# Performance work log

Measured on AMD Instinct MI355X. Metric: run time of the kernel, lower is better.

The kernel has to match this reference:

```python
import jax, jax.numpy as jnp
import numpy as np

N = 50000      # nodes
E = 600000     # edges
IN = 128       # input_dim
HID = 128      # hidden_dim
OUT = 128      # output_dim
H = 4          # heads
D = OUT // H   # head dim
R = 4          # rel_num
L = 2          # n_layer
M = 10000      # len(idx)
EPS = 1e-5


def setup_inputs() -> dict:
    key = jax.random.key(0)
    ks = jax.random.split(key, 16)
    f = jax.random.normal
    inp = {
        "x": f(ks[0], (N, IN), jnp.float32),
        "proj_w": f(ks[1], (IN, HID), jnp.float32) / np.sqrt(IN).astype(np.float32),
        "proj_b": jnp.zeros((HID,), jnp.float32),
        "bn_gamma": jnp.ones((HID,), jnp.float32),
        "bn_beta": jnp.zeros((HID,), jnp.float32),
        # per-layer HGTConv params (stacked on leading L axis; layer0 in=HID, layer1 in=OUT, equal here)
        "q_w": f(ks[2], (L, HID, OUT), jnp.float32) / np.sqrt(HID).astype(np.float32),
        "q_b": jnp.zeros((L, OUT), jnp.float32),
        "k_w": f(ks[3], (L, HID, OUT), jnp.float32) / np.sqrt(HID).astype(np.float32),
        "k_b": jnp.zeros((L, OUT), jnp.float32),
        "v_w": f(ks[4], (L, HID, OUT), jnp.float32) / np.sqrt(HID).astype(np.float32),
        "v_b": jnp.zeros((L, OUT), jnp.float32),
        "a_w": f(ks[5], (L, OUT, OUT), jnp.float32) / np.sqrt(OUT).astype(np.float32),
        "a_b": jnp.zeros((L, OUT), jnp.float32),
        "skip": jnp.ones((L,), jnp.float32),
        "a_rel": f(ks[6], (L, R, H, D, D), jnp.float32) / np.sqrt(D).astype(np.float32),
        "m_rel": f(ks[7], (L, R, H, D, D), jnp.float32) / np.sqrt(D).astype(np.float32),
        "p_rel": jnp.ones((L, R, H), jnp.float32),
        "edge_index": jax.random.randint(ks[8], (2, E), 0, N, dtype=jnp.int32),
        "edge_type": jax.random.randint(ks[9], (E,), 0, R, dtype=jnp.int32),
        "idx": jax.random.randint(ks[10], (M,), 0, N, dtype=jnp.int32),
    }
    return inp


def _hgt_forward(x, proj_w, proj_b, bn_gamma, bn_beta, q_w, q_b, k_w, k_b, v_w, v_b,
                 a_w, a_b, skip, a_rel, m_rel, p_rel, edge_index, edge_type, idx):
    # proj + BatchNorm1d (training-mode batch statistics, biased variance)
    h = x @ proj_w + proj_b
    mu = h.mean(axis=0)
    var = jnp.mean((h - mu) ** 2, axis=0)
    h = (h - mu) * jax.lax.rsqrt(var + EPS) * bn_gamma + bn_beta

    src, dst = edge_index[0], edge_index[1]          # message from src(j) to dst(i)
    seg = dst * R + edge_type                        # per-(dst, relation) softmax segments
    scale = np.float32(1.0 / np.sqrt(D))

    for l in range(L):
        q = (h @ q_w[l] + q_b[l]).reshape(N, H, D)
        k = (h @ k_w[l] + k_b[l]).reshape(N, H, D)
        v = (h @ v_w[l] + v_b[l]).reshape(N, H, D)
        # relation-specific key/value transforms for every node/relation: [N,R,H,D]
        k_all = jnp.einsum('nhd,rhde->nrhe', k, a_rel[l])
        v_all = jnp.einsum('nhd,rhde->nrhe', v, m_rel[l])
        k_e = k_all[src, edge_type]                  # [E,H,D]
        v_e = v_all[src, edge_type]                  # [E,H,D]
        score = jnp.sum(q[dst] * k_e, axis=-1) * p_rel[l][edge_type] * scale  # [E,H]
        # per-relation segment softmax over incoming edges of each dst node
        smax = jax.ops.segment_max(score, seg, num_segments=N * R)
        e = jnp.exp(score - smax[seg])
        denom = jax.ops.segment_sum(e, seg, num_segments=N * R)
        alpha = e / denom[seg]                        # [E,H]
        out = jax.ops.segment_sum(alpha[..., None] * v_e, dst, num_segments=N)
        out = out.reshape(N, OUT)
        out = jax.nn.gelu(out, approximate=False) @ a_w[l] + a_b[l]
        b = jax.nn.sigmoid(skip[l])                   # learned skip gate
        h = b * out + (1.0 - b) * h                   # dims match -> residual mix
    return h[idx]


def reference(x, proj_w, proj_b, bn_gamma, bn_beta, q_w, q_b, k_w, k_b, v_w, v_b,
              a_w, a_b, skip, a_rel, m_rel, p_rel, edge_index, edge_type, idx):
    return _hgt_forward(x, proj_w, proj_b, bn_gamma, bn_beta, q_w, q_b, k_w, k_b,
                        v_w, v_b, a_w, a_b, skip, a_rel, m_rel, p_rel,
                        edge_index, edge_type, idx)
```

## Files before the change

### kernel.cpp

```cpp
#include <hip/hip_runtime.h>
#include <math.h>

#define NN 50000
#define EE 600000
#define MOUT 10000
#define DEGCAP 384
#define NT4 (NN * 4)

typedef short bf16x8 __attribute__((ext_vector_type(8)));
typedef float f32x4 __attribute__((ext_vector_type(4)));

__device__ __forceinline__ unsigned short f2bf(float x) {
    unsigned int u = __float_as_uint(x);
    u = (u + 0x7FFFu + ((u >> 16) & 1u)) >> 16;
    return (unsigned short)u;
}
__device__ __forceinline__ float bf2f(unsigned int b) {
    return __uint_as_float(b << 16);
}

__global__ __launch_bounds__(256) void prep_kernel(
    const float* __restrict__ proj_w, const float* __restrict__ a_w,
    const float* __restrict__ q_w, const float* __restrict__ q_b,
    const float* __restrict__ a_rel,
    const float* __restrict__ k_w, const float* __restrict__ k_b,
    const float* __restrict__ v_w, const float* __restrict__ v_b,
    const float* __restrict__ m_rel, const float* __restrict__ p_rel,
    const float* __restrict__ x,
    unsigned short* __restrict__ wt_pa, unsigned short* __restrict__ qkvw,
    float* __restrict__ fbias, unsigned short* __restrict__ msg_wt,
    unsigned short* __restrict__ x_bf, int* __restrict__ cnt,
    float* __restrict__ stats)
{
    const int b = blockIdx.x, t = threadIdx.x;
    if (b < 192) {
        int wi = b >> 6;
        int flat = (b & 63) * 256 + t;
        int n = flat >> 7, c = flat & 127;
        const float* src = (wi == 0) ? proj_w : (wi == 1) ? a_w : a_w + 16384;
        wt_pa[(size_t)wi * 16384 + n * 128 + c] = f2bf(src[c * 128 + n]);
    } else if (b < 960) {
        int q = b - 192;
        int l = q >= 384 ? 1 : 0;
        int flat = (q - l * 384) * 256 + t;
        int nrow = flat >> 7, c = flat & 127;
        unsigned short* wt = qkvw + (size_t)l * 98304;
        float* fb = fbias + l * 768;
        if (nrow < 512) {
            int r = nrow >> 7, hh = (nrow >> 5) & 3, d = nrow & 31;
            float prl = p_rel[l * 16 + r * 4 + hh] * 0.17677669529663687f;
            const float* qwc = q_w + (size_t)l * 16384 + c * 128 + hh * 32;
            const float* ar  = a_rel + (size_t)(l * 4 + r) * 4096 + hh * 1024 + d * 32;
            float s = 0.f;
            #pragma unroll 8
            for (int e = 0; e < 32; ++e) s += qwc[e] * ar[e];
            wt[(size_t)nrow * 128 + c] = f2bf(s * prl);
            if (c == 0) {
                const float* qb = q_b + l * 128 + hh * 32;
                float bb = 0.f;
                #pragma unroll 8
                for (int e = 0; e < 32; ++e) bb += qb[e] * ar[e];
                fb[nrow] = bb * prl;
            }
        } else {
            int j = nrow - 512;
            int tt = j >> 2, s = j & 3;
            int col = 2 * tt + (s & 1);
            const float* w  = (s < 2) ? k_w : v_w;
            const float* bb = (s < 2) ? k_b : v_b;
            wt[(size_t)nrow * 128 + c] = f2bf(w[(size_t)l * 16384 + c * 128 + col]);
            if (c == 0) fb[nrow] = bb[l * 128 + col];
        }
    } else if (b < 1472) {
        int q = b - 960;
        int l = q >= 256 ? 1 : 0;
        int flat = (q - l * 256) * 256 + t;
        int n = flat >> 9, kk = flat & 511;
        int h = n >> 5, e = n & 31;
        int r = kk >> 7, h2 = (kk >> 5) & 3, d = kk & 31;
        float val = (h2 == h) ? m_rel[(size_t)(l * 4 + r) * 4096 + h * 1024 + d * 32 + e] : 0.f;
        msg_wt[(size_t)l * 65536 + (size_t)n * 512 + kk] = f2bf(val);
    } else if (b < 7722) {
        int i = (b - 1472) * 256 + t;
        if (i < NN * 32) {
            float4 v = ((const float4*)x)[i];
            uint2 pk;
            pk.x = (unsigned int)f2bf(v.x) | ((unsigned int)f2bf(v.y) << 16);
            pk.y = (unsigned int)f2bf(v.z) | ((unsigned int)f2bf(v.w) << 16);
            ((uint2*)x_bf)[i] = pk;
        }
    } else {
        int i = (b - 7722) * 256 + t;
        if (i < NT4) cnt[i] = 0;
        if (i < 256) stats[i] = 0.f;
    }
}

__global__ __launch_bounds__(256) void hist_kernel(const int* __restrict__ ei,
    const int* __restrict__ et, int* __restrict__ cnt, int E)
{
    int e = blockIdx.x * 256 + threadIdx.x;
    if (e < E) atomicAdd(&cnt[ei[E + e] * 4 + et[e]], 1);
}

__global__ __launch_bounds__(256) void scan_block_kernel(const int* __restrict__ cnt,
    int* __restrict__ excl, int* __restrict__ bsum, int n)
{
    __shared__ int tmp[256];
    int i = blockIdx.x * 256 + threadIdx.x;
    int v = (i < n) ? cnt[i] : 0;
    tmp[threadIdx.x] = v;
    __syncthreads();
    for (int ofs = 1; ofs < 256; ofs <<= 1) {
        int t = (threadIdx.x >= ofs) ? tmp[threadIdx.x - ofs] : 0;
        __syncthreads();
        tmp[threadIdx.x] += t;
        __syncthreads();
    }
    if (i < n) excl[i] = tmp[threadIdx.x] - v;
    if (threadIdx.x == 255) bsum[blockIdx.x] = tmp[255];
}

__global__ __launch_bounds__(256) void scan_add_kernel(int* __restrict__ excl,
    const int* __restrict__ bsum, int* __restrict__ fill,
    int* __restrict__ maskz, int n, int total)
{
    __shared__ int red[256];
    const int b = blockIdx.x;
    int partial = 0;
    for (int j = threadIdx.x; j < b; j += 256) partial += bsum[j];
    red[threadIdx.x] = partial;
    __syncthreads();
    for (int ofs = 128; ofs > 0; ofs >>= 1) {
        if (threadIdx.x < ofs) red[threadIdx.x] += red[threadIdx.x + ofs];
        __syncthreads();
    }
    int prefix = red[0];
    int i = b * 256 + threadIdx.x;
    if (i < n) {
        int o = excl[i] + prefix;
        excl[i] = o;
        fill[i] = o;
    }
    if (i < 12500) maskz[i] = 0;
    if (b == 0 && threadIdx.x == 0) excl[n] = total;
}

__global__ __launch_bounds__(256) void scatter_kernel(const int* __restrict__ ei,
    const int* __restrict__ et, int* __restrict__ fill, int* __restrict__ pack,
    const int* __restrict__ idxp, unsigned char* __restrict__ mask, int Mo, int E)
{
    int e = blockIdx.x * 256 + threadIdx.x;
    if (e >= E) return;
    int seg = ei[E + e] * 4 + et[e];
    int p = atomicAdd(&fill[seg], 1);
    pack[p] = ei[e];
    if (e < Mo) mask[idxp[e]] = 1;
}

__global__ __launch_bounds__(256) void projstats_kernel(
    const unsigned short* __restrict__ A, const unsigned short* __restrict__ Wt,
    const float* __restrict__ bias, unsigned short* __restrict__ Cb,
    float* __restrict__ stats, int M)
{
    __shared__ unsigned short As[128 * 40];
    __shared__ unsigned short Bs[128 * 40];
    const int t = threadIdx.x;
    const int wave = t >> 6, lane = t & 63;
    const int quad = lane >> 4, l16 = lane & 15;
    const int row0 = blockIdx.x * 128;
    const int wr = (wave & 1) * 64, wc = (wave >> 1) * 64;
    const int sr = t >> 1, sc = (t & 1) * 16;
    const int grow = row0 + sr;

    f32x4 acc[4][4];
    #pragma unroll
    for (int i = 0; i < 4; ++i)
        #pragma unroll
        for (int j = 0; j < 4; ++j)
            acc[i][j] = (f32x4){0.f, 0.f, 0.f, 0.f};

    uint4 av0 = make_uint4(0,0,0,0), av1 = av0, bv0, bv1;
    if (grow < M) {
        const uint4* ap = (const uint4*)(A + (size_t)grow * 128 + sc);
        av0 = ap[0]; av1 = ap[1];
    }
    {
        const uint4* bp = (const uint4*)(Wt + (size_t)sr * 128 + sc);
        bv0 = bp[0]; bv1 = bp[1];
    }
    for (int it = 0; it < 4; ++it) {
        __syncthreads();
        *(uint4*)(As + sr * 40 + sc)     = av0;
        *(uint4*)(As + sr * 40 + sc + 8) = av1;
        *(uint4*)(Bs + sr * 40 + sc)     = bv0;
        *(uint4*)(Bs + sr * 40 + sc + 8) = bv1;
        __syncthreads();
        if (it + 1 < 4) {
            int kb = (it + 1) * 32;
            if (grow < M) {
                const uint4* ap = (const uint4*)(A + (size_t)grow * 128 + kb + sc);
                av0 = ap[0]; av1 = ap[1];
            }
            const uint4* bp = (const uint4*)(Wt + (size_t)sr * 128 + kb + sc);
            bv0 = bp[0]; bv1 = bp[1];
        }
        bf16x8 af[4], bfr[4];
        #pragma unroll
        for (int f = 0; f < 4; ++f) {
            af[f]  = *(const bf16x8*)(As + (wr + f * 16 + l16) * 40 + quad * 8);
            bfr[f] = *(const bf16x8*)(Bs + (wc + f * 16 + l16) * 40 + quad * 8);
        }
        #pragma unroll
        for (int fr = 0; fr < 4; ++fr)
            #pragma unroll
            for (int fc = 0; fc < 4; ++fc)
                acc[fr][fc] = __builtin_amdgcn_mfma_f32_16x16x32_bf16(
                    af[fr], bfr[fc], acc[fr][fc], 0, 0, 0);
    }

    #pragma unroll
    for (int fc = 0; fc < 4; ++fc) {
        const int col = wc + fc * 16 + l16;
        const float bv = bias[col];
        float s = 0.f, s2 = 0.f;
        #pragma unroll
        for (int fr = 0; fr < 4; ++fr)
            #pragma unroll
            for (int reg = 0; reg < 4; ++reg) {
                int row = row0 + wr + fr * 16 + quad * 4 + reg;
                float val = acc[fr][fc][reg] + bv;
                if (row < M) {
                    Cb[(size_t)row * 128 + col] = f2bf(val);
                    s += val; s2 += val * val;
                }
            }
        s  += __shfl_xor(s, 16);  s  += __shfl_xor(s, 32);
        s2 += __shfl_xor(s2, 16); s2 += __shfl_xor(s2, 32);
        if (quad == 0) {
            atomicAdd(&stats[col], s);
            atomicAdd(&stats[128 + col], s2);
        }
    }
}

__global__ __launch_bounds__(256) void bnqkv_kernel(
    const unsigned short* __restrict__ hb, const float* __restrict__ stats,
    const float* __restrict__ gamma, const float* __restrict__ beta,
    const unsigned short* __restrict__ qkvw, const float* __restrict__ fbias,
    unsigned short* __restrict__ hn, unsigned short* __restrict__ qkv, int M)
{
    __shared__ unsigned short hS[128 * 136];
    __shared__ unsigned short Bs[128 * 40];
    __shared__ float mulS[128], addS[128];
    const int t = threadIdx.x;
    const int row0 = blockIdx.x * 128;
    if (t < 128) {
        float invN = 1.f / 50000.f;
        float mu = stats[t] * invN;
        float var = stats[128 + t] * invN - mu * mu;
        float ml = rsqrtf(var + 1e-5f) * gamma[t];
        mulS[t] = ml;
        addS[t] = beta[t] - mu * ml;
    }
    __syncthreads();
    #pragma unroll
    for (int u = 0; u < 8; ++u) {
        int li = t + u * 256;
        int row = li >> 4, c0 = (li & 15) * 8;
        uint4 pk = make_uint4(0, 0, 0, 0);
        if (row0 + row < M)
            pk = ((const uint4*)(hb + (size_t)(row0 + row) * 128))[li & 15];
        unsigned int w[4] = {pk.x, pk.y, pk.z, pk.w};
        uint4 o;
        unsigned int ov[4];
        #pragma unroll
        for (int g = 0; g < 4; ++g) {
            int c = c0 + g * 2;
            float a0 = bf2f(w[g] & 0xFFFFu) * mulS[c]     + addS[c];
            float a1 = bf2f(w[g] >> 16)     * mulS[c + 1] + addS[c + 1];
            ov[g] = (unsigned int)f2bf(a0) | ((unsigned int)f2bf(a1) << 16);
        }
        o.x = ov[0]; o.y = ov[1]; o.z = ov[2]; o.w = ov[3];
        *(uint4*)(hS + row * 136 + c0) = o;
        if (row0 + row < M)
            ((uint4*)(hn + (size_t)(row0 + row) * 128))[li & 15] = o;
    }
    __syncthreads();

    const int wave = t >> 6, lane = t & 63;
    const int quad = lane >> 4, l16 = lane & 15;
    const int wr = (wave & 1) * 64, wcl = (wave >> 1) * 64;
    const int sr = t >> 1, scc = (t & 1) * 16;
    for (int ch = 0; ch < 6; ++ch) {
        f32x4 acc[4][4];
        #pragma unroll
        for (int i = 0; i < 4; ++i)
            #pragma unroll
            for (int j = 0; j < 4; ++j)
                acc[i][j] = (f32x4){0.f, 0.f, 0.f, 0.f};
        for (int it = 0; it < 4; ++it) {
            __syncthreads();
            const uint4* bp = (const uint4*)(qkvw + (size_t)(ch * 128 + sr) * 128 + it * 32 + scc);
            *(uint4*)(Bs + sr * 40 + scc)     = bp[0];
            *(uint4*)(Bs + sr * 40 + scc + 8) = bp[1];
            __syncthreads();
            bf16x8 af[4], bfr[4];
            #pragma unroll
            for (int f = 0; f < 4; ++f) {
                af[f]  = *(const bf16x8*)(hS + (wr + f * 16 + l16) * 136 + it * 32 + quad * 8);
                bfr[f] = *(const bf16x8*)(Bs + (wcl + f * 16 + l16) * 40 + quad * 8);
            }
            #pragma unroll
            for (int fr = 0; fr < 4; ++fr)
                #pragma unroll
                for (int fc = 0; fc < 4; ++fc)
                    acc[fr][fc] = __builtin_amdgcn_mfma_f32_16x16x32_bf16(
                        af[fr], bfr[fc], acc[fr][fc], 0, 0, 0);
        }
        float b4[4];
        #pragma unroll
        for (int fc = 0; fc < 4; ++fc)
            b4[fc] = fbias[ch * 128 + wcl + fc * 16 + l16];
        #pragma unroll
        for (int fr = 0; fr < 4; ++fr)
            #pragma unroll
            for (int reg = 0; reg < 4; ++reg) {
                int row = row0 + wr + fr * 16 + quad * 4 + reg;
                if (row >= M) continue;
                #pragma unroll
                for (int fc = 0; fc < 4; ++fc) {
                    int col = ch * 128 + wcl + fc * 16 + l16;
                    qkv[(size_t)row * 768 + col] = f2bf(acc[fr][fc][reg] + b4[fc]);
                }
            }
    }
}

__global__ __launch_bounds__(256) void agg_fused_kernel(
    const unsigned short* __restrict__ qkv,
    const unsigned short* __restrict__ qbuf, int qpitch,
    const int* __restrict__ off4, const int* __restrict__ pack,
    const int* __restrict__ rowmap, unsigned short* __restrict__ aggb, int count)
{
    __shared__ int spack[4][DEGCAP];
    const int wv = threadIdx.x >> 6;
    const int lane = threadIdx.x & 63;
    const int unit = blockIdx.x * 4 + wv;
    if (unit >= count) return;
    const int node = rowmap ? __builtin_amdgcn_readfirstlane(rowmap[unit]) : unit;

    int off_r[5];
    #pragma unroll
    for (int i = 0; i < 5; ++i)
        off_r[i] = __builtin_amdgcn_readfirstlane(off4[node * 4 + i]);
    const int beg = off_r[0];
    const int deg = off_r[4] - beg;
    const bool cached = deg <= DEGCAP;

    const unsigned int* qrow = (const unsigned int*)(qbuf + (size_t)unit * qpitch);

    if (cached) {
        for (int i = lane; i < deg; i += 64) spack[wv][i] = pack[beg + i];
        asm volatile("s_waitcnt vmcnt(0) lgkmcnt(0)" ::: "memory");
    }

    unsigned int outw[4];
    for (int r = 0; r < 4; ++r) {
        unsigned int qu = qrow[r * 64 + lane];
        float qx = bf2f(qu & 0xFFFFu);
        float qy = bf2f(qu >> 16);
        float den = 0.f, ax = 0.f, ay = 0.f;

        if (cached) {
            const int rb = off_r[r] - beg, re = off_r[r + 1] - beg;
            for (int i = rb; i < re; i += 4) {
                unsigned int ku[4], vu[4];
                #pragma unroll
                for (int j = 0; j < 4; ++j) {
                    int ii = i + j; if (ii >= re) ii = re - 1;
                    int src = spack[wv][ii];
                    uint2 kv = *(const uint2*)(qkv + (size_t)src * 768 + 512 + lane * 4);
                    ku[j] = kv.x; vu[j] = kv.y;
                }
                float p[4];
                #pragma unroll
                for (int j = 0; j < 4; ++j)
                    p[j] = qx * bf2f(ku[j] & 0xFFFFu) + qy * bf2f(ku[j] >> 16);
                #pragma unroll
                for (int j = 0; j < 4; ++j) {
                    p[j] += __shfl_xor(p[j], 1); p[j] += __shfl_xor(p[j], 2);
                    p[j] += __shfl_xor(p[j], 4); p[j] += __shfl_xor(p[j], 8);
                }
                #pragma unroll
                for (int j = 0; j < 4; ++j) {
                    float s = fminf(fmaxf(p[j], -80.f), 80.f);
                    float e = __expf(s);
                    if (i + j >= re) e = 0.f;
                    den += e;
                    ax += e * bf2f(vu[j] & 0xFFFFu);
                    ay += e * bf2f(vu[j] >> 16);
                }
            }
        } else {
            for (int pp = off_r[r]; pp < off_r[r + 1]; ++pp) {
                int src = __builtin_amdgcn_readfirstlane(pack[pp]);
                uint2 kv = *(const uint2*)(qkv + (size_t)src * 768 + 512 + lane * 4);
                float p0 = qx * bf2f(kv.x & 0xFFFFu) + qy * bf2f(kv.x >> 16);
                p0 += __shfl_xor(p0, 1); p0 += __shfl_xor(p0, 2);
                p0 += __shfl_xor(p0, 4); p0 += __shfl_xor(p0, 8);
                float e = __expf(fminf(fmaxf(p0, -80.f), 80.f));
                den += e;
                ax += e * bf2f(kv.y & 0xFFFFu);
                ay += e * bf2f(kv.y >> 16);
            }
        }
        float inv = den > 0.f ? 1.f / den : 0.f;
        outw[r] = (unsigned int)f2bf(ax * inv) | ((unsigned int)f2bf(ay * inv) << 16);
    }
    unsigned int* op = (unsigned int*)(aggb + (size_t)unit * 512);
    #pragma unroll
    for (int r = 0; r < 4; ++r) op[r * 64 + lane] = outw[r];
}

__global__ __launch_bounds__(256) void mlpqkv_kernel(
    const unsigned short* __restrict__ A, const unsigned short* __restrict__ W3t,
    const unsigned short* __restrict__ AWt, const float* __restrict__ a_bias,
    const float* __restrict__ skipv, const unsigned short* __restrict__ hres,
    const unsigned short* __restrict__ qkvw1, const float* __restrict__ fbias1,
    const unsigned char* __restrict__ mask,
    unsigned short* __restrict__ h1, unsigned short* __restrict__ qkv, int M)
{
    __shared__ unsigned short As[128 * 40];
    __shared__ unsigned short Bs[128 * 40];
    __shared__ unsigned short msgS[128 * 136];
    const int t = threadIdx.x;
    const int wave = t >> 6, lane = t & 63;
    const int quad = lane >> 4, l16 = lane & 15;
    const int row0 = blockIdx.x * 128;
    const int wr = (wave & 1) * 64, wcl = (wave >> 1) * 64;
    const int sr = t >> 1, scc = (t & 1) * 16;
    const int grow = row0 + sr;
    const bool rvalid = grow < M;

    f32x4 acc[4][4];
    #pragma unroll
    for (int i = 0; i < 4; ++i)
        #pragma unroll
        for (int j = 0; j < 4; ++j)
            acc[i][j] = (f32x4){0.f, 0.f, 0.f, 0.f};

    uint4 av0 = make_uint4(0,0,0,0), av1 = av0, bv0, bv1;
    if (rvalid) {
        const uint4* ap = (const uint4*)(A + (size_t)grow * 512 + scc);
        av0 = ap[0]; av1 = ap[1];
    }
    {
        const uint4* bp = (const uint4*)(W3t + (size_t)sr * 512 + scc);
        bv0 = bp[0]; bv1 = bp[1];
    }
    for (int it = 0; it < 16; ++it) {
        __syncthreads();
        *(uint4*)(As + sr * 40 + scc)     = av0;
        *(uint4*)(As + sr * 40 + scc + 8) = av1;
        *(uint4*)(Bs + sr * 40 + scc)     = bv0;
        *(uint4*)(Bs + sr * 40 + scc + 8) = bv1;
        __syncthreads();
        if (it + 1 < 16) {
            int kb = (it + 1) * 32;
            if (rvalid) {
                const uint4* ap = (const uint4*)(A + (size_t)grow * 512 + kb + scc);
                av0 = ap[0]; av1 = ap[1];
            }
            const uint4* bp = (const uint4*)(W3t + (size_t)sr * 512 + kb + scc);
            bv0 = bp[0]; bv1 = bp[1];
        }
        bf16x8 af[4], bfr[4];
        #pragma unroll
        for (int f = 0; f < 4; ++f) {
            af[f]  = *(const bf16x8*)(As + (wr + f * 16 + l16) * 40 + quad * 8);
            bfr[f] = *(const bf16x8*)(Bs + (wcl + f * 16 + l16) * 40 + quad * 8);
        }
        #pragma unroll
        for (int fr = 0; fr < 4; ++fr)
            #pragma unroll
            for (int fc = 0; fc < 4; ++fc)
                acc[fr][fc] = __builtin_amdgcn_mfma_f32_16x16x32_bf16(
                    af[fr], bfr[fc], acc[fr][fc], 0, 0, 0);
    }

    #pragma unroll
    for (int fr = 0; fr < 4; ++fr)
        #pragma unroll
        for (int reg = 0; reg < 4; ++reg) {
            int rl = wr + fr * 16 + quad * 4 + reg;
            #pragma unroll
            for (int fc = 0; fc < 4; ++fc) {
                int col = wcl + fc * 16 + l16;
                float v = acc[fr][fc][reg];
                float gl = 0.5f * v * (1.f + erff(v * 0.70710678118654752f));
                msgS[rl * 136 + col] = f2bf(gl);
            }
        }

    f32x4 acc2[4][4];
    #pragma unroll
    for (int i = 0; i < 4; ++i)
        #pragma unroll
        for (int j = 0; j < 4; ++j)
            acc2[i][j] = (f32x4){0.f, 0.f, 0.f, 0.f};
    for (int it = 0; it < 4; ++it) {
        __syncthreads();
        const uint4* bp = (const uint4*)(AWt + (size_t)sr * 128 + it * 32 + scc);
        *(uint4*)(Bs + sr * 40 + scc)     = bp[0];
        *(uint4*)(Bs + sr * 40 + scc + 8) = bp[1];
        __syncthreads();
        bf16x8 af[4], bfr[4];
        #pragma unroll
        for (int f = 0; f < 4; ++f) {
            af[f]  = *(const bf16x8*)(msgS + (wr + f * 16 + l16) * 136 + it * 32 + quad * 8);
            bfr[f] = *(const bf16x8*)(Bs + (wcl + f * 16 + l16) * 40 + quad * 8);
        }
        #pragma unroll
        for (int fr = 0; fr < 4; ++fr)
            #pragma unroll
            for (int fc = 0; fc < 4; ++fc)
                acc2[fr][fc] = __builtin_amdgcn_mfma_f32_16x16x32_bf16(
                    af[fr], bfr[fc], acc2[fr][fc], 0, 0, 0);
    }

    const float gate = 1.f / (1.f + __expf(-skipv[0]));
    __syncthreads();
    #pragma unroll
    for (int fr = 0; fr < 4; ++fr)
        #pragma unroll
        for (int reg = 0; reg < 4; ++reg) {
            int rl = wr + fr * 16 + quad * 4 + reg;
            int row = row0 + rl;
            const bool rv = row < M;
            const bool mw = rv && mask[row];
            #pragma unroll
            for (int fc = 0; fc < 4; ++fc) {
                int col = wcl + fc * 16 + l16;
                float val = acc2[fr][fc][reg] + a_bias[col];
                float nv = val;
                if (rv) {
                    unsigned int hu = hres[(size_t)row * 128 + col];
                    nv = gate * val + (1.f - gate) * bf2f(hu);
                    if (mw) h1[(size_t)row * 128 + col] = f2bf(nv);
                }
                msgS[rl * 136 + col] = f2bf(nv);
            }
        }

    for (int ch = 4; ch < 6; ++ch) {
        f32x4 acc3[4][4];
        #pragma unroll
        for (int i = 0; i < 4; ++i)
            #pragma unroll
            for (int j = 0; j < 4; ++j)
                acc3[i][j] = (f32x4){0.f, 0.f, 0.f, 0.f};
        for (int it = 0; it < 4; ++it) {
            __syncthreads();
            const uint4* bp = (const uint4*)(qkvw1 + (size_t)(ch * 128 + sr) * 128 + it * 32 + scc);
            *(uint4*)(Bs + sr * 40 + scc)     = bp[0];
            *(uint4*)(Bs + sr * 40 + scc + 8) = bp[1];
            __syncthreads();
            bf16x8 af[4], bfr[4];
            #pragma unroll
            for (int f = 0; f < 4; ++f) {
                af[f]  = *(const bf16x8*)(msgS + (wr + f * 16 + l16) * 136 + it * 32 + quad * 8);
                bfr[f] = *(const bf16x8*)(Bs + (wcl + f * 16 + l16) * 40 + quad * 8);
            }
            #pragma unroll
            for (int fr = 0; fr < 4; ++fr)
                #pragma unroll
                for (int fc = 0; fc < 4; ++fc)
                    acc3[fr][fc] = __builtin_amdgcn_mfma_f32_16x16x32_bf16(
                        af[fr], bfr[fc], acc3[fr][fc], 0, 0, 0);
        }
        float b4[4];
        #pragma unroll
        for (int fc = 0; fc < 4; ++fc)
            b4[fc] = fbias1[ch * 128 + wcl + fc * 16 + l16];
        #pragma unroll
        for (int fr = 0; fr < 4; ++fr)
            #pragma unroll
            for (int reg = 0; reg < 4; ++reg) {
                int row = row0 + wr + fr * 16 + quad * 4 + reg;
                if (row >= M) continue;
                #pragma unroll
                for (int fc = 0; fc < 4; ++fc) {
                    int col = ch * 128 + wcl + fc * 16 + l16;
                    qkv[(size_t)row * 768 + col] = f2bf(acc3[fr][fc][reg] + b4[fc]);
                }
            }
    }
}

__global__ __launch_bounds__(256) void q1_kernel(
    const unsigned short* __restrict__ h1, const int* __restrict__ idxp,
    const unsigned short* __restrict__ qkvw1, const float* __restrict__ fbias1,
    unsigned short* __restrict__ q1, int M)
{
    __shared__ unsigned short hS[128 * 136];
    __shared__ unsigned short Bs[128 * 40];
    const int t = threadIdx.x;
    const int row0 = blockIdx.x * 128;
    #pragma unroll
    for (int u = 0; u < 8; ++u) {
        int li = t + u * 256;
        int row = li >> 4, c = li & 15;
        uint4 pk = make_uint4(0, 0, 0, 0);
        if (row0 + row < M) {
            int node = idxp[row0 + row];
            pk = ((const uint4*)(h1 + (size_t)node * 128))[c];
        }
        *(uint4*)(hS + row * 136 + c * 8) = pk;
    }
    __syncthreads();

    const int wave = t >> 6, lane = t & 63;
    const int quad = lane >> 4, l16 = lane & 15;
    const int wr = (wave & 1) * 64, wcl = (wave >> 1) * 64;
    const int sr = t >> 1, scc = (t & 1) * 16;
    for (int ch = 0; ch < 4; ++ch) {
        f32x4 acc[4][4];
        #pragma unroll
        for (int i = 0; i < 4; ++i)
            #pragma unroll
            for (int j = 0; j < 4; ++j)
                acc[i][j] = (f32x4){0.f, 0.f, 0.f, 0.f};
        for (int it = 0; it < 4; ++it) {
            __syncthreads();
            const uint4* bp = (const uint4*)(qkvw1 + (size_t)(ch * 128 + sr) * 128 + it * 32 + scc);
            *(uint4*)(Bs + sr * 40 + scc)     = bp[0];
            *(uint4*)(Bs + sr * 40 + scc + 8) = bp[1];
            __syncthreads();
            bf16x8 af[4], bfr[4];
            #pragma unroll
            for (int f = 0; f < 4; ++f) {
                af[f]  = *(const bf16x8*)(hS + (wr + f * 16 + l16) * 136 + it * 32 + quad * 8);
                bfr[f] = *(const bf16x8*)(Bs + (wcl + f * 16 + l16) * 40 + quad * 8);
            }
            #pragma unroll
            for (int fr = 0; fr < 4; ++fr)
                #pragma unroll
                for (int fc = 0; fc < 4; ++fc)
                    acc[fr][fc] = __builtin_amdgcn_mfma_f32_16x16x32_bf16(
                        af[fr], bfr[fc], acc[fr][fc], 0, 0, 0);
        }
        float b4[4];
        #pragma unroll
        for (int fc = 0; fc < 4; ++fc)
            b4[fc] = fbias1[ch * 128 + wcl + fc * 16 + l16];
        #pragma unroll
        for (int fr = 0; fr < 4; ++fr)
            #pragma unroll
            for (int reg = 0; reg < 4; ++reg) {
                int row = row0 + wr + fr * 16 + quad * 4 + reg;
                if (row >= M) continue;
                #pragma unroll
                for (int fc = 0; fc < 4; ++fc) {
                    int col = ch * 128 + wcl + fc * 16 + l16;
                    q1[(size_t)row * 512 + col] = f2bf(acc[fr][fc][reg] + b4[fc]);
                }
            }
    }
}

__global__ __launch_bounds__(256) void mlp1_kernel(
    const unsigned short* __restrict__ A, const unsigned short* __restrict__ W3t,
    const unsigned short* __restrict__ AWt, const float* __restrict__ a_bias,
    const float* __restrict__ skipv, const unsigned short* __restrict__ hres,
    const int* __restrict__ rowmap, float* __restrict__ out, int M)
{
    __shared__ unsigned short As[128 * 40];
    __shared__ unsigned short Bs[128 * 40];
    __shared__ unsigned short msgS[128 * 136];
    const int t = threadIdx.x;
    const int wave = t >> 6, lane = t & 63;
    const int quad = lane >> 4, l16 = lane & 15;
    const int row0 = blockIdx.x * 128;
    const int wr = (wave & 1) * 64, wcl = (wave >> 1) * 64;
    const int sr = t >> 1, scc = (t & 1) * 16;
    const int grow = row0 + sr;
    const bool rvalid = grow < M;

    f32x4 acc[4][4];
    #pragma unroll
    for (int i = 0; i < 4; ++i)
        #pragma unroll
        for (int j = 0; j < 4; ++j)
            acc[i][j] = (f32x4){0.f, 0.f, 0.f, 0.f};

    uint4 av0 = make_uint4(0,0,0,0), av1 = av0, bv0, bv1;
    if (rvalid) {
        const uint4* ap = (const uint4*)(A + (size_t)grow * 512 + scc);
        av0 = ap[0]; av1 = ap[1];
    }
    {
        const uint4* bp = (const uint4*)(W3t + (size_t)sr * 512 + scc);
        bv0 = bp[0]; bv1 = bp[1];
    }
    for (int it = 0; it < 16; ++it) {
        __syncthreads();
        *(uint4*)(As + sr * 40 + scc)     = av0;
        *(uint4*)(As + sr * 40 + scc + 8) = av1;
        *(uint4*)(Bs + sr * 40 + scc)     = bv0;
        *(uint4*)(Bs + sr * 40 + scc + 8) = bv1;
        __syncthreads();
        if (it + 1 < 16) {
            int kb = (it + 1) * 32;
            if (rvalid) {
                const uint4* ap = (const uint4*)(A + (size_t)grow * 512 + kb + scc);
                av0 = ap[0]; av1 = ap[1];
            }
            const uint4* bp = (const uint4*)(W3t + (size_t)sr * 512 + kb + scc);
            bv0 = bp[0]; bv1 = bp[1];
        }
        bf16x8 af[4], bfr[4];
        #pragma unroll
        for (int f = 0; f < 4; ++f) {
            af[f]  = *(const bf16x8*)(As + (wr + f * 16 + l16) * 40 + quad * 8);
            bfr[f] = *(const bf16x8*)(Bs + (wcl + f * 16 + l16) * 40 + quad * 8);
        }
        #pragma unroll
        for (int fr = 0; fr < 4; ++fr)
            #pragma unroll
            for (int fc = 0; fc < 4; ++fc)
                acc[fr][fc] = __builtin_amdgcn_mfma_f32_16x16x32_bf16(
                    af[fr], bfr[fc], acc[fr][fc], 0, 0, 0);
    }

    #pragma unroll
    for (int fr = 0; fr < 4; ++fr)
        #pragma unroll
        for (int reg = 0; reg < 4; ++reg) {
            int rl = wr + fr * 16 + quad * 4 + reg;
            #pragma unroll
            for (int fc = 0; fc < 4; ++fc) {
                int col = wcl + fc * 16 + l16;
                float v = acc[fr][fc][reg];
                float gl = 0.5f * v * (1.f + erff(v * 0.70710678118654752f));
                msgS[rl * 136 + col] = f2bf(gl);
            }
        }

    f32x4 acc2[4][4];
    #pragma unroll
    for (int i = 0; i < 4; ++i)
        #pragma unroll
        for (int j = 0; j < 4; ++j)
            acc2[i][j] = (f32x4){0.f, 0.f, 0.f, 0.f};
    for (int it = 0; it < 4; ++it) {
        __syncthreads();
        const uint4* bp = (const uint4*)(AWt + (size_t)sr * 128 + it * 32 + scc);
        *(uint4*)(Bs + sr * 40 + scc)     = bp[0];
        *(uint4*)(Bs + sr * 40 + scc + 8) = bp[1];
        __syncthreads();
        bf16x8 af[4], bfr[4];
        #pragma unroll
        for (int f = 0; f < 4; ++f) {
            af[f]  = *(const bf16x8*)(msgS + (wr + f * 16 + l16) * 136 + it * 32 + quad * 8);
            bfr[f] = *(const bf16x8*)(Bs + (wcl + f * 16 + l16) * 40 + quad * 8);
        }
        #pragma unroll
        for (int fr = 0; fr < 4; ++fr)
            #pragma unroll
            for (int fc = 0; fc < 4; ++fc)
                acc2[fr][fc] = __builtin_amdgcn_mfma_f32_16x16x32_bf16(
                    af[fr], bfr[fc], acc2[fr][fc], 0, 0, 0);
    }

    const float gate = 1.f / (1.f + __expf(-skipv[0]));
    #pragma unroll
    for (int fr = 0; fr < 4; ++fr)
        #pragma unroll
        for (int reg = 0; reg < 4; ++reg) {
            int row = row0 + wr + fr * 16 + quad * 4 + reg;
            if (row >= M) continue;
            int hrow = rowmap[row];
            #pragma unroll
            for (int fc = 0; fc < 4; ++fc) {
                int col = wcl + fc * 16 + l16;
                float val = acc2[fr][fc][reg] + a_bias[col];
                float nv = gate * val + (1.f - gate) * bf2f((unsigned int)hres[(size_t)hrow * 128 + col]);
                out[(size_t)row * 128 + col] = nv;
            }
        }
}

extern "C" void kernel_launch(void* const* d_in, const int* in_sizes, int n_in,
                              void* d_out, int out_size, void* d_ws, size_t ws_size,
                              hipStream_t stream)
{
    const float* x      = (const float*)d_in[0];
    const float* proj_w = (const float*)d_in[1];
    const float* proj_b = (const float*)d_in[2];
    const float* bn_g   = (const float*)d_in[3];
    const float* bn_b   = (const float*)d_in[4];
    const float* q_w    = (const float*)d_in[5];
    const float* q_b    = (const float*)d_in[6];
    const float* k_w    = (const float*)d_in[7];
    const float* k_b    = (const float*)d_in[8];
    const float* v_w    = (const float*)d_in[9];
    const float* v_b    = (const float*)d_in[10];
    const float* a_w    = (const float*)d_in[11];
    const float* a_b    = (const float*)d_in[12];
    const float* skip   = (const float*)d_in[13];
    const float* a_rel  = (const float*)d_in[14];
    const float* m_rel  = (const float*)d_in[15];
    const float* p_rel  = (const float*)d_in[16];
    const int* edge_index = (const int*)d_in[17];
    const int* edge_type  = (const int*)d_in[18];
    const int* idx        = (const int*)d_in[19];
    float* out = (float*)d_out;

    const int N = NN, E = EE;
    float* ws = (float*)d_ws;
    size_t o = 0;
    float* stats  = ws + o;  o += 256;
    float* fbias  = ws + o;  o += 2 * 768;
    int* cnt  = (int*)(ws + o); o += NT4;
    int* off4 = (int*)(ws + o); o += NT4 + 1;
    int* fill = (int*)(ws + o); o += NT4;
    int* bsum = (int*)(ws + o); o += 1024;
    int* pack = (int*)(ws + o); o += E;
    unsigned short* x_bf   = (unsigned short*)(ws + o); o += (size_t)N * 64;
    unsigned short* h_bf   = (unsigned short*)(ws + o); o += (size_t)N * 64;
    unsigned short* hn_bf  = (unsigned short*)(ws + o); o += (size_t)N * 64;
    unsigned short* h1_bf  = (unsigned short*)(ws + o); o += (size_t)N * 64;
    unsigned short* qkv_bf = (unsigned short*)(ws + o); o += (size_t)N * 384;
    unsigned short* agg_bf = (unsigned short*)(ws + o); o += (size_t)N * 256;
    unsigned short* wt_pa  = (unsigned short*)(ws + o); o += 3 * 16384 / 2;
    unsigned short* qkvw   = (unsigned short*)(ws + o); o += 2 * 98304 / 2;
    unsigned short* msg_wt = (unsigned short*)(ws + o); o += 2 * 65536 / 2;

    unsigned char* mask = (unsigned char*)cnt;
    unsigned short* q1 = x_bf;

    const int NB4 = (NT4 + 255) / 256;
    const int g = (N + 127) / 128;

    prep_kernel<<<7722 + NB4, 256, 0, stream>>>(
        proj_w, a_w, q_w, q_b, a_rel, k_w, k_b, v_w, v_b, m_rel, p_rel, x,
        wt_pa, qkvw, fbias, msg_wt, x_bf, cnt, stats);

    hist_kernel<<<(E + 255) / 256, 256, 0, stream>>>(edge_index, edge_type, cnt, E);
    scan_block_kernel<<<NB4, 256, 0, stream>>>(cnt, off4, bsum, NT4);
    scan_add_kernel<<<NB4, 256, 0, stream>>>(off4, bsum, fill, cnt, NT4, E);
    scatter_kernel<<<(E + 255) / 256, 256, 0, stream>>>(edge_index, edge_type, fill,
                                                        pack, idx, mask, MOUT, E);

    projstats_kernel<<<g, 256, 0, stream>>>(x_bf, wt_pa, proj_b, h_bf, stats, N);

    bnqkv_kernel<<<g, 256, 0, stream>>>(h_bf, stats, bn_g, bn_b, qkvw, fbias,
                                        hn_bf, qkv_bf, N);

    agg_fused_kernel<<<(N + 3) / 4, 256, 0, stream>>>(qkv_bf, qkv_bf, 768,
                                                      off4, pack, nullptr, agg_bf, N);

    mlpqkv_kernel<<<g, 256, 0, stream>>>(agg_bf, msg_wt, wt_pa + 16384, a_b, skip,
                                         hn_bf, qkvw + 98304, fbias + 768,
                                         mask, h1_bf, qkv_bf, N);

    q1_kernel<<<(MOUT + 127) / 128, 256, 0, stream>>>(h1_bf, idx, qkvw + 98304,
                                                      fbias + 768, q1, MOUT);

    agg_fused_kernel<<<(MOUT + 3) / 4, 256, 0, stream>>>(qkv_bf, q1, 512,
                                                         off4, pack, idx, agg_bf, MOUT);

    mlp1_kernel<<<(MOUT + 127) / 128, 256, 0, stream>>>(agg_bf, msg_wt + 65536,
                                                        wt_pa + 2 * 16384, a_b + 128,
                                                        skip + 1, h1_bf, idx, out, MOUT);
}
```

Before: 454.9 us.

## Prefetch GEMM weight tiles into registers and use persistent atomic work-stealing aggregation

The MFMA GEMM loops in the bnqkv, mlpqkv, q1 and mlp1 kernels now load the next weight K-slice into registers while the current slice is being computed, so global load latency overlaps with the MFMAs. The edge aggregation kernel becomes persistent: a fixed grid of waves pulls two nodes at a time from an atomic counter, which balances uneven node degrees. The counters are zeroed inside the scan kernel using spare bsum slots. This adds atomic contention and extra register pressure from the prefetched tiles.

```diff
diff --git a/kernel.cpp b/kernel.cpp
--- a/kernel.cpp
+++ b/kernel.cpp
@@ -107,6 +107,7 @@
     int* __restrict__ excl, int* __restrict__ bsum, int n)
 {
     __shared__ int tmp[256];
+    if (blockIdx.x == 0 && threadIdx.x == 0) { bsum[1000] = 0; bsum[1001] = 0; }
     int i = blockIdx.x * 256 + threadIdx.x;
     int v = (i < n) ? cnt[i] : 0;
     tmp[threadIdx.x] = v;
@@ -292,6 +293,12 @@
     const int quad = lane >> 4, l16 = lane & 15;
     const int wr = (wave & 1) * 64, wcl = (wave >> 1) * 64;
     const int sr = t >> 1, scc = (t & 1) * 16;
+
+    uint4 pv0, pv1;
+    {
+        const uint4* bp = (const uint4*)(qkvw + (size_t)sr * 128 + scc);
+        pv0 = bp[0]; pv1 = bp[1];
+    }
     for (int ch = 0; ch < 6; ++ch) {
         f32x4 acc[4][4];
         #pragma unroll
@@ -301,10 +308,15 @@
                 acc[i][j] = (f32x4){0.f, 0.f, 0.f, 0.f};
         for (int it = 0; it < 4; ++it) {
             __syncthreads();
-            const uint4* bp = (const uint4*)(qkvw + (size_t)(ch * 128 + sr) * 128 + it * 32 + scc);
-            *(uint4*)(Bs + sr * 40 + scc)     = bp[0];
-            *(uint4*)(Bs + sr * 40 + scc + 8) = bp[1];
+            *(uint4*)(Bs + sr * 40 + scc)     = pv0;
+            *(uint4*)(Bs + sr * 40 + scc + 8) = pv1;
             __syncthreads();
+            int nit = it + 1, nch = ch;
+            if (nit == 4) { nit = 0; ++nch; }
+            if (nch < 6) {
+                const uint4* bp = (const uint4*)(qkvw + (size_t)(nch * 128 + sr) * 128 + nit * 32 + scc);
+                pv0 = bp[0]; pv1 = bp[1];
+            }
             bf16x8 af[4], bfr[4];
             #pragma unroll
             for (int f = 0; f < 4; ++f) {
@@ -341,86 +353,94 @@
     const unsigned short* __restrict__ qkv,
     const unsigned short* __restrict__ qbuf, int qpitch,
     const int* __restrict__ off4, const int* __restrict__ pack,
-    const int* __restrict__ rowmap, unsigned short* __restrict__ aggb, int count)
+    const int* __restrict__ rowmap, unsigned short* __restrict__ aggb,
+    int* __restrict__ ctr, int count)
 {
     __shared__ int spack[4][DEGCAP];
     const int wv = threadIdx.x >> 6;
     const int lane = threadIdx.x & 63;
-    const int unit = blockIdx.x * 4 + wv;
-    if (unit >= count) return;
-    const int node = rowmap ? __builtin_amdgcn_readfirstlane(rowmap[unit]) : unit;
-
-    int off_r[5];
-    #pragma unroll
-    for (int i = 0; i < 5; ++i)
-        off_r[i] = __builtin_amdgcn_readfirstlane(off4[node * 4 + i]);
-    const int beg = off_r[0];
-    const int deg = off_r[4] - beg;
-    const bool cached = deg <= DEGCAP;
-
-    const unsigned int* qrow = (const unsigned int*)(qbuf + (size_t)unit * qpitch);
-
-    if (cached) {
-        for (int i = lane; i < deg; i += 64) spack[wv][i] = pack[beg + i];
-        asm volatile("s_waitcnt vmcnt(0) lgkmcnt(0)" ::: "memory");
-    }
-
-    unsigned int outw[4];
-    for (int r = 0; r < 4; ++r) {
-        unsigned int qu = qrow[r * 64 + lane];
-        float qx = bf2f(qu & 0xFFFFu);
-        float qy = bf2f(qu >> 16);
-        float den = 0.f, ax = 0.f, ay = 0.f;
-
-        if (cached) {
-            const int rb = off_r[r] - beg, re = off_r[r + 1] - beg;
-            for (int i = rb; i < re; i += 4) {
-                unsigned int ku[4], vu[4];
-                #pragma unroll
-                for (int j = 0; j < 4; ++j) {
-                    int ii = i + j; if (ii >= re) ii = re - 1;
-                    int src = spack[wv][ii];
-                    uint2 kv = *(const uint2*)(qkv + (size_t)src * 768 + 512 + lane * 4);
-                    ku[j] = kv.x; vu[j] = kv.y;
+    for (;;) {
+        int u0 = 0;
+        if (lane == 0) u0 = atomicAdd(ctr, 2);
+        u0 = __shfl(u0, 0);
+        if (u0 >= count) break;
+        const int uend = (u0 + 2 < count) ? u0 + 2 : count;
+        for (int unit = u0; unit < uend; ++unit) {
+            const int node = rowmap ? __builtin_amdgcn_readfirstlane(rowmap[unit]) : unit;
+
+            int off_r[5];
+            #pragma unroll
+            for (int i = 0; i < 5; ++i)
+                off_r[i] = __builtin_amdgcn_readfirstlane(off4[node * 4 + i]);
+            const int beg = off_r[0];
+            const int deg = off_r[4] - beg;
+            const bool cached = deg <= DEGCAP;
+
+            const unsigned int* qrow = (const unsigned int*)(qbuf + (size_t)unit * qpitch);
+
+            if (cached) {
+                for (int i = lane; i < deg; i += 64) spack[wv][i] = pack[beg + i];
+                asm volatile("s_waitcnt vmcnt(0) lgkmcnt(0)" ::: "memory");
+            }
+
+            unsigned int outw[4];
+            for (int r = 0; r < 4; ++r) {
+                unsigned int qu = qrow[r * 64 + lane];
+                float qx = bf2f(qu & 0xFFFFu);
+                float qy = bf2f(qu >> 16);
+                float den = 0.f, ax = 0.f, ay = 0.f;
+
+                if (cached) {
+                    const int rb = off_r[r] - beg, re = off_r[r + 1] - beg;
+                    for (int i = rb; i < re; i += 4) {
+                        unsigned int ku[4], vu[4];
+                        #pragma unroll
+                        for (int j = 0; j < 4; ++j) {
+                            int ii = i + j; if (ii >= re) ii = re - 1;
+                            int src = spack[wv][ii];
+                            uint2 kv = *(const uint2*)(qkv + (size_t)src * 768 + 512 + lane * 4);
+                            ku[j] = kv.x; vu[j] = kv.y;
+                        }
+                        float p[4];
+                        #pragma unroll
+                        for (int j = 0; j < 4; ++j)
+                            p[j] = qx * bf2f(ku[j] & 0xFFFFu) + qy * bf2f(ku[j] >> 16);
+                        #pragma unroll
+                        for (int j = 0; j < 4; ++j) {
+                            p[j] += __shfl_xor(p[j], 1); p[j] += __shfl_xor(p[j], 2);
+                            p[j] += __shfl_xor(p[j], 4); p[j] += __shfl_xor(p[j], 8);
+                        }
+                        #pragma unroll
+                        for (int j = 0; j < 4; ++j) {
+                            float s = fminf(fmaxf(p[j], -80.f), 80.f);
+                            float e = __expf(s);
+                            if (i + j >= re) e = 0.f;
+                            den += e;
+                            ax += e * bf2f(vu[j] & 0xFFFFu);
+                            ay += e * bf2f(vu[j] >> 16);
+                        }
+                    }
+                } else {
+                    for (int pp = off_r[r]; pp < off_r[r + 1]; ++pp) {
+                        int src = __builtin_amdgcn_readfirstlane(pack[pp]);
+                        uint2 kv = *(const uint2*)(qkv + (size_t)src * 768 + 512 + lane * 4);
+                        float p0 = qx * bf2f(kv.x & 0xFFFFu) + qy * bf2f(kv.x >> 16);
+                        p0 += __shfl_xor(p0, 1); p0 += __shfl_xor(p0, 2);
+                        p0 += __shfl_xor(p0, 4); p0 += __shfl_xor(p0, 8);
+                        float e = __expf(fminf(fmaxf(p0, -80.f), 80.f));
+                        den += e;
+                        ax += e * bf2f(kv.y & 0xFFFFu);
+                        ay += e * bf2f(kv.y >> 16);
+                    }
                 }
-                float p[4];
-                #pragma unroll
-                for (int j = 0; j < 4; ++j)
-                    p[j] = qx * bf2f(ku[j] & 0xFFFFu) + qy * bf2f(ku[j] >> 16);
-                #pragma unroll
-                for (int j = 0; j < 4; ++j) {
-                    p[j] += __shfl_xor(p[j], 1); p[j] += __shfl_xor(p[j], 2);
-                    p[j] += __shfl_xor(p[j], 4); p[j] += __shfl_xor(p[j], 8);
-                }
-                #pragma unroll
-                for (int j = 0; j < 4; ++j) {
-                    float s = fminf(fmaxf(p[j], -80.f), 80.f);
-                    float e = __expf(s);
-                    if (i + j >= re) e = 0.f;
-                    den += e;
-                    ax += e * bf2f(vu[j] & 0xFFFFu);
-                    ay += e * bf2f(vu[j] >> 16);
-                }
-            }
-        } else {
-            for (int pp = off_r[r]; pp < off_r[r + 1]; ++pp) {
-                int src = __builtin_amdgcn_readfirstlane(pack[pp]);
-                uint2 kv = *(const uint2*)(qkv + (size_t)src * 768 + 512 + lane * 4);
-                float p0 = qx * bf2f(kv.x & 0xFFFFu) + qy * bf2f(kv.x >> 16);
-                p0 += __shfl_xor(p0, 1); p0 += __shfl_xor(p0, 2);
-                p0 += __shfl_xor(p0, 4); p0 += __shfl_xor(p0, 8);
-                float e = __expf(fminf(fmaxf(p0, -80.f), 80.f));
-                den += e;
-                ax += e * bf2f(kv.y & 0xFFFFu);
-                ay += e * bf2f(kv.y >> 16);
-            }
-        }
-        float inv = den > 0.f ? 1.f / den : 0.f;
-        outw[r] = (unsigned int)f2bf(ax * inv) | ((unsigned int)f2bf(ay * inv) << 16);
-    }
-    unsigned int* op = (unsigned int*)(aggb + (size_t)unit * 512);
-    #pragma unroll
-    for (int r = 0; r < 4; ++r) op[r * 64 + lane] = outw[r];
+                float inv = den > 0.f ? 1.f / den : 0.f;
+                outw[r] = (unsigned int)f2bf(ax * inv) | ((unsigned int)f2bf(ay * inv) << 16);
+            }
+            unsigned int* op = (unsigned int*)(aggb + (size_t)unit * 512);
+            #pragma unroll
+            for (int r = 0; r < 4; ++r) op[r * 64 + lane] = outw[r];
+        }
+    }
 }
 
 __global__ __launch_bounds__(256) void mlpqkv_kernel(
@@ -509,12 +529,23 @@
         #pragma unroll
         for (int j = 0; j < 4; ++j)
             acc2[i][j] = (f32x4){0.f, 0.f, 0.f, 0.f};
+    uint4 pv0, pv1;
+    {
+        const uint4* bp = (const uint4*)(AWt + (size_t)sr * 128 + scc);
+        pv0 = bp[0]; pv1 = bp[1];
+    }
     for (int it = 0; it < 4; ++it) {
         __syncthreads();
-        const uint4* bp = (const uint4*)(AWt + (size_t)sr * 128 + it * 32 + scc);
-        *(uint4*)(Bs + sr * 40 + scc)     = bp[0];
-        *(uint4*)(Bs + sr * 40 + scc + 8) = bp[1];
-        __syncthreads();
+        *(uint4*)(Bs + sr * 40 + scc)     = pv0;
+        *(uint4*)(Bs + sr * 40 + scc + 8) = pv1;
+        __syncthreads();
+        if (it + 1 < 4) {
+            const uint4* bp = (const uint4*)(AWt + (size_t)sr * 128 + (it + 1) * 32 + scc);
+            pv0 = bp[0]; pv1 = bp[1];
+        } else {
+            const uint4* bp = (const uint4*)(qkvw1 + (size_t)(4 * 128 + sr) * 128 + scc);
+            pv0 = bp[0]; pv1 = bp[1];
+        }
         bf16x8 af[4], bfr[4];
         #pragma unroll
         for (int f = 0; f < 4; ++f) {
@@ -562,10 +593,15 @@
                 acc3[i][j] = (f32x4){0.f, 0.f, 0.f, 0.f};
         for (int it = 0; it < 4; ++it) {
             __syncthreads();
-            const uint4* bp = (const uint4*)(qkvw1 + (size_t)(ch * 128 + sr) * 128 + it * 32 + scc);
-            *(uint4*)(Bs + sr * 40 + scc)     = bp[0];
-            *(uint4*)(Bs + sr * 40 + scc + 8) = bp[1];
+            *(uint4*)(Bs + sr * 40 + scc)     = pv0;
+            *(uint4*)(Bs + sr * 40 + scc + 8) = pv1;
             __syncthreads();
+            int nit = it + 1, nch = ch;
+            if (nit == 4) { nit = 0; ++nch; }
+            if (nch < 6) {
+                const uint4* bp = (const uint4*)(qkvw1 + (size_t)(nch * 128 + sr) * 128 + nit * 32 + scc);
+                pv0 = bp[0]; pv1 = bp[1];
+            }
             bf16x8 af[4], bfr[4];
             #pragma unroll
             for (int f = 0; f < 4; ++f) {
@@ -624,6 +660,11 @@
     const int quad = lane >> 4, l16 = lane & 15;
     const int wr = (wave & 1) * 64, wcl = (wave >> 1) * 64;
     const int sr = t >> 1, scc = (t & 1) * 16;
+    uint4 pv0, pv1;
+    {
+        const uint4* bp = (const uint4*)(qkvw1 + (size_t)sr * 128 + scc);
+        pv0 = bp[0]; pv1 = bp[1];
+    }
     for (int ch = 0; ch < 4; ++ch) {
         f32x4 acc[4][4];
         #pragma unroll
@@ -633,10 +674,15 @@
                 acc[i][j] = (f32x4){0.f, 0.f, 0.f, 0.f};
         for (int it = 0; it < 4; ++it) {
             __syncthreads();
-            const uint4* bp = (const uint4*)(qkvw1 + (size_t)(ch * 128 + sr) * 128 + it * 32 + scc);
-            *(uint4*)(Bs + sr * 40 + scc)     = bp[0];
-            *(uint4*)(Bs + sr * 40 + scc + 8) = bp[1];
+            *(uint4*)(Bs + sr * 40 + scc)     = pv0;
+            *(uint4*)(Bs + sr * 40 + scc + 8) = pv1;
             __syncthreads();
+            int nit = it + 1, nch = ch;
+            if (nit == 4) { nit = 0; ++nch; }
+            if (nch < 4) {
+                const uint4* bp = (const uint4*)(qkvw1 + (size_t)(nch * 128 + sr) * 128 + nit * 32 + scc);
+                pv0 = bp[0]; pv1 = bp[1];
+            }
             bf16x8 af[4], bfr[4];
             #pragma unroll
             for (int f = 0; f < 4; ++f) {
@@ -753,12 +799,20 @@
         #pragma unroll
         for (int j = 0; j < 4; ++j)
             acc2[i][j] = (f32x4){0.f, 0.f, 0.f, 0.f};
+    uint4 pv0, pv1;
+    {
+        const uint4* bp = (const uint4*)(AWt + (size_t)sr * 128 + scc);
+        pv0 = bp[0]; pv1 = bp[1];
+    }
     for (int it = 0; it < 4; ++it) {
         __syncthreads();
-        const uint4* bp = (const uint4*)(AWt + (size_t)sr * 128 + it * 32 + scc);
-        *(uint4*)(Bs + sr * 40 + scc)     = bp[0];
-        *(uint4*)(Bs + sr * 40 + scc + 8) = bp[1];
-        __syncthreads();
+        *(uint4*)(Bs + sr * 40 + scc)     = pv0;
+        *(uint4*)(Bs + sr * 40 + scc + 8) = pv1;
+        __syncthreads();
+        if (it + 1 < 4) {
+            const uint4* bp = (const uint4*)(AWt + (size_t)sr * 128 + (it + 1) * 32 + scc);
+            pv0 = bp[0]; pv1 = bp[1];
+        }
         bf16x8 af[4], bfr[4];
         #pragma unroll
         for (int f = 0; f < 4; ++f) {
@@ -839,6 +893,8 @@
 
     unsigned char* mask = (unsigned char*)cnt;
     unsigned short* q1 = x_bf;
+    int* ctr0 = bsum + 1000;
+    int* ctr1 = bsum + 1001;
 
     const int NB4 = (NT4 + 255) / 256;
     const int g = (N + 127) / 128;
@@ -858,8 +914,8 @@
     bnqkv_kernel<<<g, 256, 0, stream>>>(h_bf, stats, bn_g, bn_b, qkvw, fbias,
                                         hn_bf, qkv_bf, N);
 
-    agg_fused_kernel<<<(N + 3) / 4, 256, 0, stream>>>(qkv_bf, qkv_bf, 768,
-                                                      off4, pack, nullptr, agg_bf, N);
+    agg_fused_kernel<<<2048, 256, 0, stream>>>(qkv_bf, qkv_bf, 768,
+                                               off4, pack, nullptr, agg_bf, ctr0, N);
 
     mlpqkv_kernel<<<g, 256, 0, stream>>>(agg_bf, msg_wt, wt_pa + 16384, a_b, skip,
                                          hn_bf, qkvw + 98304, fbias + 768,
@@ -868,8 +924,8 @@
     q1_kernel<<<(MOUT + 127) / 128, 256, 0, stream>>>(h1_bf, idx, qkvw + 98304,
                                                       fbias + 768, q1, MOUT);
 
-    agg_fused_kernel<<<(MOUT + 3) / 4, 256, 0, stream>>>(qkv_bf, q1, 512,
-                                                         off4, pack, idx, agg_bf, MOUT);
+    agg_fused_kernel<<<1024, 256, 0, stream>>>(qkv_bf, q1, 512,
+                                               off4, pack, idx, agg_bf, ctr1, MOUT);
 
     mlp1_kernel<<<(MOUT + 127) / 128, 256, 0, stream>>>(agg_bf, msg_wt + 65536,
                                                         wt_pa + 2 * 16384, a_b + 128,
```

Result: slower. 870.8 us (+91.4%).
